# Kernel optimization log

Measured on AMD Instinct MI355X. Metric: run time of the kernel, lower is better.

The kernel has to match this reference:

```python
import jax, jax.numpy as jnp
import numpy as np

EPS = 1e-6


def setup_inputs() -> dict:
    key = jax.random.key(0)
    k1, k2 = jax.random.split(key)
    T, B, D, n = 2048, 16, 1024, 64
    x = jax.random.normal(k1, (T, B, D), dtype=jnp.float32)
    S0 = jnp.zeros((B, n, n), dtype=jnp.float32)
    G0 = jnp.zeros((B, n, n), dtype=jnp.float32)
    # xavier-uniform-ish init for each n x D block of the fused projection
    limit = float(np.sqrt(6.0 / (n + D)))
    W_kvqm = jax.random.uniform(k2, (4 * n, D), dtype=jnp.float32, minval=-limit, maxval=limit)
    b_s_gate = jnp.full((n,), 2.0, dtype=jnp.float32)
    b_g_gate = jnp.full((n,), 2.5, dtype=jnp.float32)
    return {"x": x, "S0": S0, "G0": G0, "W_kvqm": W_kvqm,
            "b_s_gate": b_s_gate, "b_g_gate": b_g_gate}


def _e81_forward(x, S0, G0, W_kvqm, b_s_gate, b_g_gate):
    T, B, D = x.shape
    n = b_s_gate.shape[0]
    # Fused projection: [T, B, 4n]
    proj = jnp.einsum('tbd,nd->tbn', x, W_kvqm)
    k_all, v_all, q_all, m_all = jnp.split(proj, 4, axis=-1)

    bs = b_s_gate[None, :, None]  # broadcast over [B, n(row), n(col)]
    bg = b_g_gate[None, :, None]

    def step(carry, kvqm):
        S, G = carry
        k, v, q, m_vec = kvqm  # each [B, n]
        k_norm = k / (jnp.linalg.norm(k, axis=-1, keepdims=True) + EPS)
        m_norm = m_vec / (jnp.linalg.norm(m_vec, axis=-1, keepdims=True) + EPS)

        gate_S = jax.nn.sigmoid(G + bs)
        s_retrieved = jnp.einsum('bij,bj->bi', S, k_norm)
        s_delta = v - s_retrieved
        S = gate_S * S + jnp.einsum('bi,bj->bij', s_delta, k_norm)

        gate_G = jax.nn.sigmoid(S + bg)
        g_retrieved = jnp.einsum('bij,bj->bi', G, m_norm)
        g_delta = s_delta - g_retrieved
        G = gate_G * G + jnp.einsum('bi,bj->bij', g_delta, m_norm)

        Sq = jnp.einsum('bij,bj->bi', S, q)
        out = Sq * jax.nn.silu(Sq)  # self-gated output
        return (S, G), out

    (S, G), output = jax.lax.scan(step, (S0, G0), (k_all, v_all, q_all, m_all))
    return output, S, G


def reference(x, S0, G0, W_kvqm, b_s_gate, b_g_gate):
    return _e81_forward(x, S0, G0, W_kvqm, b_s_gate, b_g_gate)
```

## Files before the change

kernel.cpp:

```cpp
#include <hip/hip_runtime.h>
#include <hip/hip_bf16.h>

#define EPS 1e-6f
#define L2E 1.4426950408889634f

typedef float f32x4 __attribute__((ext_vector_type(4)));
typedef short bf16x8 __attribute__((ext_vector_type(8)));

template <int CTRL>
__device__ __forceinline__ float dpp_mov(float v) {
  return __int_as_float(
      __builtin_amdgcn_update_dpp(0, __float_as_int(v), CTRL, 0xF, 0xF, true));
}

__device__ __forceinline__ float reduce16(float v) {
  v += dpp_mov<0x121>(v);
  v += dpp_mov<0x122>(v);
  v += dpp_mov<0x124>(v);
  v += dpp_mov<0x128>(v);
  return v;
}

__device__ __forceinline__ float reduce64_all(float v) {
  v = reduce16(v);
#if __has_builtin(__builtin_amdgcn_permlane16_swap) && \
    __has_builtin(__builtin_amdgcn_permlane32_swap)
  {
    auto r = __builtin_amdgcn_permlane16_swap(__float_as_int(v),
                                              __float_as_int(v), false, false);
    v = __int_as_float(r[0]) + __int_as_float(r[1]);
  }
  {
    auto r = __builtin_amdgcn_permlane32_swap(__float_as_int(v),
                                              __float_as_int(v), false, false);
    v = __int_as_float(r[0]) + __int_as_float(r[1]);
  }
  return v;
#else
  v += dpp_mov<0x142>(v);
  v += dpp_mov<0x143>(v);
  return __int_as_float(__builtin_amdgcn_readlane(__float_as_int(v), 63));
#endif
}

__device__ __forceinline__ float sigm_b(float x, float nb) {
  float t = __builtin_amdgcn_exp2f(fmaf(x, -L2E, nb));
  return __builtin_amdgcn_rcpf(1.0f + t);
}
__device__ __forceinline__ float sigm(float x) {
  float t = __builtin_amdgcn_exp2f(x * -L2E);
  return __builtin_amdgcn_rcpf(1.0f + t);
}

__device__ __forceinline__ unsigned f2bf(float x) {
  __hip_bfloat16 h = __float2bfloat16(x);
  return *reinterpret_cast<unsigned short*>(&h);
}
__device__ __forceinline__ unsigned split_pack(float x) {
  unsigned hi = f2bf(x);
  unsigned short hs = (unsigned short)hi;
  float hif = __bfloat162float(*reinterpret_cast<__hip_bfloat16*>(&hs));
  unsigned lo = f2bf(x - hif);
  return (lo << 16) | hi;
}

union FragCast { unsigned u[4]; bf16x8 v; };

constexpr int GBM = 128, GBK = 32;

__global__ __launch_bounds__(512) void proj_gemm_mfma(
    const float* __restrict__ A,
    const float* __restrict__ Bw,
    float* __restrict__ C,
    int M, int K) {
  __shared__ unsigned As[GBM * GBK];
  __shared__ unsigned Bs[256 * GBK];

  const int tid  = threadIdx.x;
  const int lane = tid & 63;
  const int wid  = tid >> 6;
  const int m0   = blockIdx.x * GBM;
  const int wm   = (wid >> 2) * 64;
  const int wn   = (wid & 3) * 64;

  const int ar = tid >> 2, ak = (tid & 3) * 8;
  const int br = tid >> 1, bk = (tid & 1) * 16;

  f32x4 acc[4][4] = {};

  for (int k0 = 0; k0 < K; k0 += GBK) {
    {
      const float* src = &A[(size_t)(m0 + ar) * K + k0 + ak];
      float4 v0 = *(const float4*)(src);
      float4 v1 = *(const float4*)(src + 4);
      unsigned p0[4] = {split_pack(v0.x), split_pack(v0.y),
                        split_pack(v0.z), split_pack(v0.w)};
      unsigned p1[4] = {split_pack(v1.x), split_pack(v1.y),
                        split_pack(v1.z), split_pack(v1.w)};
      unsigned swz  = (unsigned)(ar & 7) << 4;
      char* base = (char*)As + ar * 128;
      *(uint4*)(base + (((unsigned)ak * 4) ^ swz))       = *(uint4*)p0;
      *(uint4*)(base + (((unsigned)(ak + 4) * 4) ^ swz)) = *(uint4*)p1;
    }
    {
      const float* src = &Bw[(size_t)br * K + k0 + bk];
      unsigned swz = (unsigned)(br & 7) << 4;
      char* base = (char*)Bs + br * 128;
#pragma unroll
      for (int q = 0; q < 4; ++q) {
        float4 v = *(const float4*)(src + q * 4);
        unsigned p[4] = {split_pack(v.x), split_pack(v.y),
                         split_pack(v.z), split_pack(v.w)};
        *(uint4*)(base + (((unsigned)(bk + q * 4) * 4) ^ swz)) = *(uint4*)p;
      }
    }
    __syncthreads();

    unsigned ah[4][4], al[4][4];
    const unsigned ko = ((unsigned)(lane >> 4)) * 16;
#pragma unroll
    for (int mf = 0; mf < 4; ++mf) {
      int r = wm + mf * 16 + (lane & 15);
      unsigned swz = (unsigned)(r & 7) << 4;
      char* base = (char*)As + r * 128;
      uint4 w0 = *(uint4*)(base + (ko ^ swz));
      uint4 w1 = *(uint4*)(base + ((64 + ko) ^ swz));
      ah[mf][0] = __builtin_amdgcn_perm(w0.y, w0.x, 0x05040100);
      al[mf][0] = __builtin_amdgcn_perm(w0.y, w0.x, 0x07060302);
      ah[mf][1] = __builtin_amdgcn_perm(w0.w, w0.z, 0x05040100);
      al[mf][1] = __builtin_amdgcn_perm(w0.w, w0.z, 0x07060302);
      ah[mf][2] = __builtin_amdgcn_perm(w1.y, w1.x, 0x05040100);
      al[mf][2] = __builtin_amdgcn_perm(w1.y, w1.x, 0x07060302);
      ah[mf][3] = __builtin_amdgcn_perm(w1.w, w1.z, 0x05040100);
      al[mf][3] = __builtin_amdgcn_perm(w1.w, w1.z, 0x07060302);
    }

#pragma unroll
    for (int nf = 0; nf < 4; ++nf) {
      int r = wn + nf * 16 + (lane & 15);
      unsigned swz = (unsigned)(r & 7) << 4;
      char* base = (char*)Bs + r * 128;
      uint4 w0 = *(uint4*)(base + (ko ^ swz));
      uint4 w1 = *(uint4*)(base + ((64 + ko) ^ swz));
      FragCast bh, bl;
      bh.u[0] = __builtin_amdgcn_perm(w0.y, w0.x, 0x05040100);
      bl.u[0] = __builtin_amdgcn_perm(w0.y, w0.x, 0x07060302);
      bh.u[1] = __builtin_amdgcn_perm(w0.w, w0.z, 0x05040100);
      bl.u[1] = __builtin_amdgcn_perm(w0.w, w0.z, 0x07060302);
      bh.u[2] = __builtin_amdgcn_perm(w1.y, w1.x, 0x05040100);
      bl.u[2] = __builtin_amdgcn_perm(w1.y, w1.x, 0x07060302);
      bh.u[3] = __builtin_amdgcn_perm(w1.w, w1.z, 0x05040100);
      bl.u[3] = __builtin_amdgcn_perm(w1.w, w1.z, 0x07060302);
#pragma unroll
      for (int mf = 0; mf < 4; ++mf) {
        FragCast fah, fal;
        fah.u[0] = ah[mf][0]; fah.u[1] = ah[mf][1];
        fah.u[2] = ah[mf][2]; fah.u[3] = ah[mf][3];
        fal.u[0] = al[mf][0]; fal.u[1] = al[mf][1];
        fal.u[2] = al[mf][2]; fal.u[3] = al[mf][3];
        acc[mf][nf] = __builtin_amdgcn_mfma_f32_16x16x32_bf16(
            fah.v, bh.v, acc[mf][nf], 0, 0, 0);
        acc[mf][nf] = __builtin_amdgcn_mfma_f32_16x16x32_bf16(
            fah.v, bl.v, acc[mf][nf], 0, 0, 0);
        acc[mf][nf] = __builtin_amdgcn_mfma_f32_16x16x32_bf16(
            fal.v, bh.v, acc[mf][nf], 0, 0, 0);
      }
    }
    __syncthreads();
  }

  float rn[4][4];
  const int wcol = wid & 3;
  if (wcol == 0 || wcol == 3) {
#pragma unroll
    for (int mf = 0; mf < 4; ++mf)
#pragma unroll
      for (int r = 0; r < 4; ++r) {
        float ss = acc[mf][0][r] * acc[mf][0][r];
        ss = fmaf(acc[mf][1][r], acc[mf][1][r], ss);
        ss = fmaf(acc[mf][2][r], acc[mf][2][r], ss);
        ss = fmaf(acc[mf][3][r], acc[mf][3][r], ss);
        ss = reduce16(ss);
        rn[mf][r] = __builtin_amdgcn_rcpf(sqrtf(ss) + EPS);
      }
  } else {
#pragma unroll
    for (int mf = 0; mf < 4; ++mf)
#pragma unroll
      for (int r = 0; r < 4; ++r) rn[mf][r] = 1.0f;
  }

#pragma unroll
  for (int mf = 0; mf < 4; ++mf) {
    int row = m0 + wm + mf * 16 + (lane >> 4) * 4;
#pragma unroll
    for (int nf = 0; nf < 4; ++nf) {
      int col = wn + nf * 16 + (lane & 15);
#pragma unroll
      for (int r = 0; r < 4; ++r)
        C[(size_t)(row + r) * 256 + col] = acc[mf][nf][r] * rn[mf][r];
    }
  }
}

#define PSTR 4096

__global__ __launch_bounds__(256) void e81_scan(
    const float* __restrict__ proj,
    const float* __restrict__ S0,
    const float* __restrict__ G0,
    const float* __restrict__ bsg,
    const float* __restrict__ bgg,
    float* __restrict__ dout,
    int T) {
  const int lane = threadIdx.x & 63;
  const int wave = threadIdx.x >> 6;
  const int b    = blockIdx.x >> 4;
  const int row  = ((blockIdx.x & 15) << 2) + wave;

  const size_t sgi = ((size_t)(b * 64 + row)) * 64 + lane;
  float S = S0[sgi];
  float G = G0[sgi];
  const float nbs = -bsg[row] * L2E;
  const float nbg = -bgg[row] * L2E;

  float* outp = dout;
  float* Sout = dout + (size_t)T * 16 * 64;
  float* Gout = Sout + 16 * 64 * 64;

  const float* pA = proj + b * 256;
  const float* pB = pA + PSTR;
  float kA = pA[lane], qA = pA[128 + lane], mA = pA[192 + lane], vA = pA[64 + row];
  float kB = pB[lane], qB = pB[128 + lane], mB = pB[192 + lane], vB = pB[64 + row];

#define STEP(k_, q_, m_, v_, tidx)                                   \
  {                                                                  \
    float gs = sigm_b(G, nbs);                \
    float sr = reduce64_all(S * k_);                                 \
    float gr = reduce64_all(G * m_);                                 \
    float sdelta = v_ - sr;                                          \
    S = fmaf(gs, S, sdelta * k_);                                    \
    float sq = reduce64_all(S * q_);                                 \
    float gg = sigm_b(S, nbg);                                       \
    G = fmaf(gg, G, (sdelta - gr) * m_);                             \
    if (lane == 0) outp[(((size_t)(tidx) << 4) + b) * 64 + row] = sq;\
  }

  for (int t = 0; t < T; t += 2) {
    const float* pA2 = (t + 2 < T) ? (pA + 2 * PSTR) : pA;
    const float* pB2 = (t + 3 < T) ? (pB + 2 * PSTR) : pB;
    float kA2 = pA2[lane], qA2 = pA2[128 + lane], mA2 = pA2[192 + lane],
          vA2 = pA2[64 + row];
    float kB2 = pB2[lane], qB2 = pB2[128 + lane], mB2 = pB2[192 + lane],
          vB2 = pB2[64 + row];

    STEP(kA, qA, mA, vA, t)
    STEP(kB, qB, mB, vB, t + 1)

    kA = kA2; qA = qA2; mA = mA2; vA = vA2; pA = pA2;
    kB = kB2; qB = qB2; mB = mB2; vB = vB2; pB = pB2;
  }
#undef STEP

  Sout[sgi] = S;
  Gout[sgi] = G;
}

__global__ __launch_bounds__(256) void out_act(float* __restrict__ o, int n4) {
  int i = blockIdx.x * 256 + threadIdx.x;
  if (i < n4) {
    float4 x = *(float4*)(o + 4 * i);
    float4 r;
    r.x = x.x * x.x * sigm(x.x);
    r.y = x.y * x.y * sigm(x.y);
    r.z = x.z * x.z * sigm(x.z);
    r.w = x.w * x.w * sigm(x.w);
    *(float4*)(o + 4 * i) = r;
  }
}

extern "C" void kernel_launch(void* const* d_in, const int* in_sizes, int n_in,
                              void* d_out, int out_size, void* d_ws, size_t ws_size,
                              hipStream_t stream) {
  const float* x  = (const float*)d_in[0];
  const float* S0 = (const float*)d_in[1];
  const float* G0 = (const float*)d_in[2];
  const float* W  = (const float*)d_in[3];
  const float* bs = (const float*)d_in[4];
  const float* bg = (const float*)d_in[5];
  float* out = (float*)d_out;
  float* proj = (float*)d_ws;

  const int B = 16, D = 1024;
  const int T = in_sizes[0] / (B * D);
  const int M = T * B;

  proj_gemm_mfma<<<dim3(M / GBM), 512, 0, stream>>>(x, W, proj, M, D);

  e81_scan<<<dim3(256), 256, 0, stream>>>(proj, S0, G0, bs, bg, out, T);

  const int n4 = T * B * 64 / 4;
  out_act<<<dim3((n4 + 255) / 256), 256, 0, stream>>>(out, n4);
}
```

Measured before the change: 772.6 us.

## Prepack W to split-bf16 tiles, widen GEMM K-tile, deepen scan prefetch and regroup blocks

A new kernel splits W into hi/lo bf16 pairs once, stores them in a pre-swizzled tiled layout inside the output buffer, and has the GEMM copy those tiles straight into LDS instead of converting W in every block. The bf16 split now truncates instead of rounding, the GEMM K-tile grows from 32 to 64 so there are half as many barriers, and the scan kernel prefetches three steps deep with a scheduling barrier. The scan also runs 8 waves per block over 128 blocks with a permuted block-to-row mapping. Risks are a small precision change from truncation and the extra w_pack launch; using d_out as scratch is safe only because the GEMM finishes before the scan writes the output.

Measured after the change: 759.0 us. No clear change (-1.8%).

```diff
diff --git a/kernel.cpp b/kernel.cpp
--- a/kernel.cpp
+++ b/kernel.cpp
@@ -52,25 +52,33 @@
   return __builtin_amdgcn_rcpf(1.0f + t);
 }
 
-__device__ __forceinline__ unsigned f2bf(float x) {
-  __hip_bfloat16 h = __float2bfloat16(x);
-  return *reinterpret_cast<unsigned short*>(&h);
-}
-__device__ __forceinline__ unsigned split_pack(float x) {
-  unsigned hi = f2bf(x);
-  unsigned short hs = (unsigned short)hi;
-  float hif = __bfloat162float(*reinterpret_cast<__hip_bfloat16*>(&hs));
-  unsigned lo = f2bf(x - hif);
-  return (lo << 16) | hi;
+__device__ __forceinline__ unsigned split_pack_fast(float x) {
+  float hi = __int_as_float(__float_as_int(x) & 0xFFFF0000u);
+  float lo = x - hi;
+  return __builtin_amdgcn_perm(__float_as_int(lo), __float_as_int(x),
+                               0x07060302);
 }
 
 union FragCast { unsigned u[4]; bf16x8 v; };
 
-constexpr int GBM = 128, GBK = 32;
+__global__ __launch_bounds__(256) void w_pack(const float* __restrict__ W,
+                                              unsigned* __restrict__ Wpk) {
+  int idx = blockIdx.x * 256 + threadIdx.x;
+  int r = idx >> 10;
+  int k = idx & 1023;
+  unsigned p = split_pack_fast(W[idx]);
+  int tile = k >> 6, kt = k & 63;
+  unsigned byte = (unsigned)tile * 65536u + (unsigned)r * 256u +
+                  ((((unsigned)kt >> 2) * 16u) ^ (((unsigned)r & 7u) << 4)) +
+                  ((unsigned)kt & 3u) * 4u;
+  *(unsigned*)((char*)Wpk + byte) = p;
+}
+
+constexpr int GBM = 128, GBK = 64;
 
 __global__ __launch_bounds__(512) void proj_gemm_mfma(
     const float* __restrict__ A,
-    const float* __restrict__ Bw,
+    const unsigned* __restrict__ Wpk,
     float* __restrict__ C,
     int M, int K) {
   __shared__ unsigned As[GBM * GBK];
@@ -83,87 +91,83 @@
   const int wm   = (wid >> 2) * 64;
   const int wn   = (wid & 3) * 64;
 
-  const int ar = tid >> 2, ak = (tid & 3) * 8;
-  const int br = tid >> 1, bk = (tid & 1) * 16;
+  const int ar = tid >> 2, ak = (tid & 3) * 16;
 
   f32x4 acc[4][4] = {};
 
-  for (int k0 = 0; k0 < K; k0 += GBK) {
+  for (int t8 = 0; t8 < K / GBK; ++t8) {
+    const int k0 = t8 * GBK;
     {
       const float* src = &A[(size_t)(m0 + ar) * K + k0 + ak];
-      float4 v0 = *(const float4*)(src);
-      float4 v1 = *(const float4*)(src + 4);
-      unsigned p0[4] = {split_pack(v0.x), split_pack(v0.y),
-                        split_pack(v0.z), split_pack(v0.w)};
-      unsigned p1[4] = {split_pack(v1.x), split_pack(v1.y),
-                        split_pack(v1.z), split_pack(v1.w)};
-      unsigned swz  = (unsigned)(ar & 7) << 4;
-      char* base = (char*)As + ar * 128;
-      *(uint4*)(base + (((unsigned)ak * 4) ^ swz))       = *(uint4*)p0;
-      *(uint4*)(base + (((unsigned)(ak + 4) * 4) ^ swz)) = *(uint4*)p1;
+      unsigned swz = (unsigned)(ar & 7) << 4;
+      char* base = (char*)As + ar * 256;
+#pragma unroll
+      for (int q = 0; q < 4; ++q) {
+        float4 v = *(const float4*)(src + q * 4);
+        unsigned p[4] = {split_pack_fast(v.x), split_pack_fast(v.y),
+                         split_pack_fast(v.z), split_pack_fast(v.w)};
+        *(uint4*)(base + (((unsigned)(ak + q * 4) * 4) ^ swz)) = *(uint4*)p;
+      }
     }
     {
-      const float* src = &Bw[(size_t)br * K + k0 + bk];
-      unsigned swz = (unsigned)(br & 7) << 4;
-      char* base = (char*)Bs + br * 128;
-#pragma unroll
-      for (int q = 0; q < 4; ++q) {
-        float4 v = *(const float4*)(src + q * 4);
-        unsigned p[4] = {split_pack(v.x), split_pack(v.y),
-                         split_pack(v.z), split_pack(v.w)};
-        *(uint4*)(base + (((unsigned)(bk + q * 4) * 4) ^ swz)) = *(uint4*)p;
-      }
+      const char* gsrc = (const char*)Wpk + (size_t)t8 * 65536 + tid * 16;
+      char* ldst = (char*)Bs + tid * 16;
+#pragma unroll
+      for (int i = 0; i < 8; ++i)
+        *(uint4*)(ldst + i * 8192) = *(const uint4*)(gsrc + i * 8192);
     }
     __syncthreads();
 
-    unsigned ah[4][4], al[4][4];
-    const unsigned ko = ((unsigned)(lane >> 4)) * 16;
-#pragma unroll
-    for (int mf = 0; mf < 4; ++mf) {
-      int r = wm + mf * 16 + (lane & 15);
-      unsigned swz = (unsigned)(r & 7) << 4;
-      char* base = (char*)As + r * 128;
-      uint4 w0 = *(uint4*)(base + (ko ^ swz));
-      uint4 w1 = *(uint4*)(base + ((64 + ko) ^ swz));
-      ah[mf][0] = __builtin_amdgcn_perm(w0.y, w0.x, 0x05040100);
-      al[mf][0] = __builtin_amdgcn_perm(w0.y, w0.x, 0x07060302);
-      ah[mf][1] = __builtin_amdgcn_perm(w0.w, w0.z, 0x05040100);
-      al[mf][1] = __builtin_amdgcn_perm(w0.w, w0.z, 0x07060302);
-      ah[mf][2] = __builtin_amdgcn_perm(w1.y, w1.x, 0x05040100);
-      al[mf][2] = __builtin_amdgcn_perm(w1.y, w1.x, 0x07060302);
-      ah[mf][3] = __builtin_amdgcn_perm(w1.w, w1.z, 0x05040100);
-      al[mf][3] = __builtin_amdgcn_perm(w1.w, w1.z, 0x07060302);
-    }
-
-#pragma unroll
-    for (int nf = 0; nf < 4; ++nf) {
-      int r = wn + nf * 16 + (lane & 15);
-      unsigned swz = (unsigned)(r & 7) << 4;
-      char* base = (char*)Bs + r * 128;
-      uint4 w0 = *(uint4*)(base + (ko ^ swz));
-      uint4 w1 = *(uint4*)(base + ((64 + ko) ^ swz));
-      FragCast bh, bl;
-      bh.u[0] = __builtin_amdgcn_perm(w0.y, w0.x, 0x05040100);
-      bl.u[0] = __builtin_amdgcn_perm(w0.y, w0.x, 0x07060302);
-      bh.u[1] = __builtin_amdgcn_perm(w0.w, w0.z, 0x05040100);
-      bl.u[1] = __builtin_amdgcn_perm(w0.w, w0.z, 0x07060302);
-      bh.u[2] = __builtin_amdgcn_perm(w1.y, w1.x, 0x05040100);
-      bl.u[2] = __builtin_amdgcn_perm(w1.y, w1.x, 0x07060302);
-      bh.u[3] = __builtin_amdgcn_perm(w1.w, w1.z, 0x05040100);
-      bl.u[3] = __builtin_amdgcn_perm(w1.w, w1.z, 0x07060302);
+#pragma unroll
+    for (int g = 0; g < 2; ++g) {
+      unsigned ah[4][4], al[4][4];
+      const unsigned ko = g * 128 + ((unsigned)(lane >> 4)) * 16;
 #pragma unroll
       for (int mf = 0; mf < 4; ++mf) {
-        FragCast fah, fal;
-        fah.u[0] = ah[mf][0]; fah.u[1] = ah[mf][1];
-        fah.u[2] = ah[mf][2]; fah.u[3] = ah[mf][3];
-        fal.u[0] = al[mf][0]; fal.u[1] = al[mf][1];
-        fal.u[2] = al[mf][2]; fal.u[3] = al[mf][3];
-        acc[mf][nf] = __builtin_amdgcn_mfma_f32_16x16x32_bf16(
-            fah.v, bh.v, acc[mf][nf], 0, 0, 0);
-        acc[mf][nf] = __builtin_amdgcn_mfma_f32_16x16x32_bf16(
-            fah.v, bl.v, acc[mf][nf], 0, 0, 0);
-        acc[mf][nf] = __builtin_amdgcn_mfma_f32_16x16x32_bf16(
-            fal.v, bh.v, acc[mf][nf], 0, 0, 0);
+        int r = wm + mf * 16 + (lane & 15);
+        unsigned swz = (unsigned)(r & 7) << 4;
+        char* base = (char*)As + r * 256;
+        uint4 w0 = *(uint4*)(base + (ko ^ swz));
+        uint4 w1 = *(uint4*)(base + ((64 + ko) ^ swz));
+        ah[mf][0] = __builtin_amdgcn_perm(w0.y, w0.x, 0x05040100);
+        al[mf][0] = __builtin_amdgcn_perm(w0.y, w0.x, 0x07060302);
+        ah[mf][1] = __builtin_amdgcn_perm(w0.w, w0.z, 0x05040100);
+        al[mf][1] = __builtin_amdgcn_perm(w0.w, w0.z, 0x07060302);
+        ah[mf][2] = __builtin_amdgcn_perm(w1.y, w1.x, 0x05040100);
+        al[mf][2] = __builtin_amdgcn_perm(w1.y, w1.x, 0x07060302);
+        ah[mf][3] = __builtin_amdgcn_perm(w1.w, w1.z, 0x05040100);
+        al[mf][3] = __builtin_amdgcn_perm(w1.w, w1.z, 0x07060302);
+      }
+#pragma unroll
+      for (int nf = 0; nf < 4; ++nf) {
+        int r = wn + nf * 16 + (lane & 15);
+        unsigned swz = (unsigned)(r & 7) << 4;
+        char* base = (char*)Bs + r * 256;
+        uint4 w0 = *(uint4*)(base + (ko ^ swz));
+        uint4 w1 = *(uint4*)(base + ((64 + ko) ^ swz));
+        FragCast bh, bl;
+        bh.u[0] = __builtin_amdgcn_perm(w0.y, w0.x, 0x05040100);
+        bl.u[0] = __builtin_amdgcn_perm(w0.y, w0.x, 0x07060302);
+        bh.u[1] = __builtin_amdgcn_perm(w0.w, w0.z, 0x05040100);
+        bl.u[1] = __builtin_amdgcn_perm(w0.w, w0.z, 0x07060302);
+        bh.u[2] = __builtin_amdgcn_perm(w1.y, w1.x, 0x05040100);
+        bl.u[2] = __builtin_amdgcn_perm(w1.y, w1.x, 0x07060302);
+        bh.u[3] = __builtin_amdgcn_perm(w1.w, w1.z, 0x05040100);
+        bl.u[3] = __builtin_amdgcn_perm(w1.w, w1.z, 0x07060302);
+#pragma unroll
+        for (int mf = 0; mf < 4; ++mf) {
+          FragCast fah, fal;
+          fah.u[0] = ah[mf][0]; fah.u[1] = ah[mf][1];
+          fah.u[2] = ah[mf][2]; fah.u[3] = ah[mf][3];
+          fal.u[0] = al[mf][0]; fal.u[1] = al[mf][1];
+          fal.u[2] = al[mf][2]; fal.u[3] = al[mf][3];
+          acc[mf][nf] = __builtin_amdgcn_mfma_f32_16x16x32_bf16(
+              fah.v, bh.v, acc[mf][nf], 0, 0, 0);
+          acc[mf][nf] = __builtin_amdgcn_mfma_f32_16x16x32_bf16(
+              fah.v, bl.v, acc[mf][nf], 0, 0, 0);
+          acc[mf][nf] = __builtin_amdgcn_mfma_f32_16x16x32_bf16(
+              fal.v, bh.v, acc[mf][nf], 0, 0, 0);
+        }
       }
     }
     __syncthreads();
@@ -205,7 +209,7 @@
 
 #define PSTR 4096
 
-__global__ __launch_bounds__(256) void e81_scan(
+__global__ __launch_bounds__(512) void e81_scan(
     const float* __restrict__ proj,
     const float* __restrict__ S0,
     const float* __restrict__ G0,
@@ -213,10 +217,13 @@
     const float* __restrict__ bgg,
     float* __restrict__ dout,
     int T) {
+  const int L = (blockIdx.x & 7) * 16 + (blockIdx.x >> 3);
+  const int w = L * 8 + (threadIdx.x >> 6);
   const int lane = threadIdx.x & 63;
-  const int wave = threadIdx.x >> 6;
-  const int b    = blockIdx.x >> 4;
-  const int row  = ((blockIdx.x & 15) << 2) + wave;
+  const int b   = w >> 6;
+  const int row = w & 63;
+  const int Tm1 = T - 1;
+  const int bo  = b * 256;
 
   const size_t sgi = ((size_t)(b * 64 + row)) * 64 + lane;
   float S = S0[sgi];
@@ -228,39 +235,55 @@
   float* Sout = dout + (size_t)T * 16 * 64;
   float* Gout = Sout + 16 * 64 * 64;
 
-  const float* pA = proj + b * 256;
-  const float* pB = pA + PSTR;
-  float kA = pA[lane], qA = pA[128 + lane], mA = pA[192 + lane], vA = pA[64 + row];
-  float kB = pB[lane], qB = pB[128 + lane], mB = pB[192 + lane], vB = pB[64 + row];
-
-#define STEP(k_, q_, m_, v_, tidx)                                   \
-  {                                                                  \
-    float gs = sigm_b(G, nbs);                \
-    float sr = reduce64_all(S * k_);                                 \
-    float gr = reduce64_all(G * m_);                                 \
-    float sdelta = v_ - sr;                                          \
-    S = fmaf(gs, S, sdelta * k_);                                    \
-    float sq = reduce64_all(S * q_);                                 \
-    float gg = sigm_b(S, nbg);                                       \
-    G = fmaf(gg, G, (sdelta - gr) * m_);                             \
-    if (lane == 0) outp[(((size_t)(tidx) << 4) + b) * 64 + row] = sq;\
-  }
-
-  for (int t = 0; t < T; t += 2) {
-    const float* pA2 = (t + 2 < T) ? (pA + 2 * PSTR) : pA;
-    const float* pB2 = (t + 3 < T) ? (pB + 2 * PSTR) : pB;
-    float kA2 = pA2[lane], qA2 = pA2[128 + lane], mA2 = pA2[192 + lane],
-          vA2 = pA2[64 + row];
-    float kB2 = pB2[lane], qB2 = pB2[128 + lane], mB2 = pB2[192 + lane],
-          vB2 = pB2[64 + row];
-
-    STEP(kA, qA, mA, vA, t)
-    STEP(kB, qB, mB, vB, t + 1)
-
-    kA = kA2; qA = qA2; mA = mA2; vA = vA2; pA = pA2;
-    kB = kB2; qB = qB2; mB = mB2; vB = vB2; pB = pB2;
-  }
+#define DECLB(n) float kA##n, qA##n, mA##n, vA##n, kB##n, qB##n, mB##n, vB##n;
+#define LOADB(n, tt)                                                        \
+  {                                                                         \
+    int _ta = (tt) < Tm1 ? (tt) : Tm1;                                      \
+    int _tb = (tt) + 1 < Tm1 ? (tt) + 1 : Tm1;                              \
+    const float* _pa = proj + (size_t)_ta * PSTR + bo;                      \
+    const float* _pb = proj + (size_t)_tb * PSTR + bo;                      \
+    kA##n = _pa[lane]; qA##n = _pa[128 + lane];                             \
+    mA##n = _pa[192 + lane]; vA##n = _pa[64 + row];                         \
+    kB##n = _pb[lane]; qB##n = _pb[128 + lane];                             \
+    mB##n = _pb[192 + lane]; vB##n = _pb[64 + row];                         \
+  }
+
+#define STEP(k_, q_, m_, v_, tidx)                                          \
+  {                                                                         \
+    float gs = sigm_b(G, nbs);                                              \
+    float sr = reduce64_all(S * k_);                                        \
+    float gr = reduce64_all(G * m_);                                        \
+    float sdelta = v_ - sr;                                                 \
+    S = fmaf(gs, S, sdelta * k_);                                           \
+    float sq = reduce64_all(S * q_);                                        \
+    float gg = sigm_b(S, nbg);                                              \
+    G = fmaf(gg, G, (sdelta - gr) * m_);                                    \
+    if (lane == 0) outp[(((size_t)(tidx) << 4) + b) * 64 + row] = sq;       \
+  }
+
+#define BODY(nc, ni, tt)                                                    \
+  LOADB(ni, (tt) + 4)                                                       \
+  __builtin_amdgcn_sched_barrier(0);                                        \
+  STEP(kA##nc, qA##nc, mA##nc, vA##nc, (tt))                                \
+  STEP(kB##nc, qB##nc, mB##nc, vB##nc, (tt) + 1)
+
+  DECLB(0) DECLB(1) DECLB(2)
+  LOADB(0, 0)
+  LOADB(1, 2)
+
+  int t = 0;
+  for (; t + 8 <= T; t += 6) {
+    BODY(0, 2, t)
+    BODY(1, 0, t + 2)
+    BODY(2, 1, t + 4)
+  }
+  STEP(kA0, qA0, mA0, vA0, t)
+  STEP(kB0, qB0, mB0, vB0, t + 1)
+
+#undef BODY
 #undef STEP
+#undef LOADB
+#undef DECLB
 
   Sout[sgi] = S;
   Gout[sgi] = G;
@@ -290,14 +313,17 @@
   const float* bg = (const float*)d_in[5];
   float* out = (float*)d_out;
   float* proj = (float*)d_ws;
+  unsigned* Wpk = (unsigned*)d_out;
 
   const int B = 16, D = 1024;
   const int T = in_sizes[0] / (B * D);
   const int M = T * B;
 
-  proj_gemm_mfma<<<dim3(M / GBM), 512, 0, stream>>>(x, W, proj, M, D);
-
-  e81_scan<<<dim3(256), 256, 0, stream>>>(proj, S0, G0, bs, bg, out, T);
+  w_pack<<<dim3(256 * 1024 / 256), 256, 0, stream>>>(W, Wpk);
+
+  proj_gemm_mfma<<<dim3(M / GBM), 512, 0, stream>>>(x, Wpk, proj, M, D);
+
+  e81_scan<<<dim3(128), 512, 0, stream>>>(proj, S0, G0, bs, bg, out, T);
 
   const int n4 = T * B * 64 / 4;
   out_act<<<dim3((n4 + 255) / 256), 256, 0, stream>>>(out, n4);
```
